# Kernel tuning notes

Hardware: AMD Instinct MI355X
Metric: run time of the kernel (lower is better)

## Reference

```python
import jax, jax.numpy as jnp
import numpy as np
from jax import lax

STRIDE = (1, 1)
PADDING = ((1, 1), (1, 1))
DILATION = (1, 1)
GROUPS = 1


def setup_inputs() -> dict:
    key = jax.random.key(0)
    k1, k2, k3, k4, k5 = jax.random.split(key, 5)
    # quantized int8-ish activations/weights stored as float (as in the torch module)
    x = jax.random.randint(k1, (32, 128, 56, 56), -128, 128).astype(jnp.float32)
    weight_int = jax.random.randint(k2, (256, 128, 3, 3), -128, 128).astype(jnp.float32)
    bias_int = jax.random.randint(k3, (256,), -1024, 1024).astype(jnp.float32)
    A = jax.random.randint(k4, (256,), 1, 32768)  # per-channel requant multiplier
    N = jax.random.randint(k5, (256,), 16, 25)    # per-channel shift
    return {
        "x": x,
        "weight_int": weight_int,
        "bias_int": bias_int,
        "A": A,
        "N": N,
        "out_min": 0,
        "out_max": 255,
    }


def reference(x, weight_int, bias_int, A, N, out_min, out_max):
    # emulate torch's x.int().float() truncation casts
    xq = jnp.trunc(x)
    wq = jnp.trunc(weight_int)
    bq = jnp.trunc(bias_int)
    out = lax.conv_general_dilated(
        xq, wq,
        window_strides=STRIDE,
        padding=PADDING,
        rhs_dilation=DILATION,
        feature_group_count=GROUPS,
        dimension_numbers=("NCHW", "OIHW", "NCHW"),
    )
    out = jnp.round(out + bq[None, :, None, None])
    # out *= A ; out >>= N  (torch float rshift == divide by 2**N)
    Af = A.astype(jnp.float32)[None, :, None, None]
    Nf = N.astype(jnp.float32)[None, :, None, None]
    out = out * Af / jnp.exp2(Nf)
    if out_min >= 0:
        out = jnp.clip(jnp.round(out), float(out_min), float(out_max))
    return out
```

## Files before the change

### kernel.cpp

```cpp
#include <hip/hip_runtime.h>
#include <stdint.h>

typedef int   v4i __attribute__((ext_vector_type(4)));
typedef float v4f __attribute__((ext_vector_type(4)));

#define XT_H_STRIDE (66*128)
#define XT_N_STRIDE (58*66*128)
#define XT_BYTES    (32*58*66*128)
#define WQ_BYTES    (256*1152)

__device__ __forceinline__ void gload16(const void* g, void* l) {
  __builtin_amdgcn_global_load_lds(
      (const __attribute__((address_space(1))) void*)g,
      (__attribute__((address_space(3))) void*)l, 16, 0, 0);
}

__global__ __launch_bounds__(256) void xform_x(const float* __restrict__ x,
                                               char* __restrict__ xt) {
  __shared__ int LB[56 * 33];
  int bid = blockIdx.x;
  int n  = bid / 58;
  int hp = bid - n * 58;
  int t  = threadIdx.x;
  int srch = hp - 1;
  bool rowok = (srch >= 0) && (srch < 56);
  char* dstrow = xt + (size_t)n * XT_N_STRIDE + (size_t)hp * XT_H_STRIDE;

  if (rowok) {
    const float* rb = x + ((size_t)(n * 128) * 56 + srch) * 56;
#pragma unroll
    for (int u0 = 0; u0 < 2; ++u0) {
      int u  = t + u0 * 256;
      int wb = u & 15;
      int cb = u >> 4;
      int w0 = wb * 4, ci0 = cb * 4;
      if (w0 < 56) {
        int dw[4] = {0, 0, 0, 0};
#pragma unroll
        for (int i = 0; i < 4; ++i) {
          v4f f = *(const v4f*)(rb + (size_t)(ci0 + i) * 3136 + w0);
#pragma unroll
          for (int j = 0; j < 4; ++j)
            dw[j] |= (((int)f[j]) & 255) << (8 * i);
        }
#pragma unroll
        for (int j = 0; j < 4; ++j)
          LB[(w0 + j) * 33 + cb] = dw[j];
      }
    }
    __syncthreads();
    for (int c = t; c < 528; c += 256) {
      int wp  = c >> 3;
      int cio = c & 7;
      int srw = wp - 1;
      v4i v = {0, 0, 0, 0};
      if (srw >= 0 && srw < 56) {
#pragma unroll
        for (int k = 0; k < 4; ++k) v[k] = LB[srw * 33 + cio * 4 + k];
      }
      *(v4i*)(dstrow + c * 16) = v;
    }
  } else {
    v4i z = {0, 0, 0, 0};
    for (int c = t; c < 528; c += 256) *(v4i*)(dstrow + c * 16) = z;
  }
}

__global__ __launch_bounds__(256) void xform_w(const float* __restrict__ wsrc,
                                               const int* __restrict__ Aq,
                                               const int* __restrict__ Nq,
                                               char* __restrict__ wq2,
                                               float* __restrict__ scale) {
  int idx = blockIdx.x * 256 + threadIdx.x;
  int co = idx / 1152;
  int k  = idx - co * 1152;
  int g  = k >> 7;
  int ci = k & 127;
  int kh = g / 3;
  int kw = g - 3 * kh;
  float f = wsrc[(size_t)(co * 128 + ci) * 9 + kh * 3 + kw];
  wq2[((k >> 6) * 256 + co) * 64 + (k & 63)] = (signed char)(int)f;
  if (idx < 256) {
    scale[idx] = (float)Aq[idx] * exp2f(-(float)Nq[idx]);
  }
}

__global__ __launch_bounds__(256, 3) void qconv_gemm(
    const char* __restrict__ xt, const char* __restrict__ wq2,
    const float* __restrict__ bias, const float* __restrict__ scale,
    const int* __restrict__ pmin, const int* __restrict__ pmax,
    float* __restrict__ out) {
  __shared__ __align__(16) char Bp[4 * 8448];

  int bid = blockIdx.x;
  int xcd = bid & 7;
  int q   = bid >> 3;
  int mt  = q & 1;
  int nt  = xcd * 112 + (q >> 1);
  int n   = nt / 28;
  int ht  = nt - n * 28;
  int h0  = ht * 2;
  int m0  = mt * 128;

  int t  = threadIdx.x;
  int wv = t >> 6;
  int ln = t & 63;
  int quad = ln >> 4;
  int l16  = ln & 15;
  int wm = wv & 1, wn = wv >> 1;

  const char* xb = xt + (size_t)n * XT_N_STRIDE + (size_t)h0 * XT_H_STRIDE;

  const char* abase = wq2 + (size_t)(m0 + wm * 64 + l16) * 64 + quad * 16;

  v4i areg[2][4];
#pragma unroll
  for (int i = 0; i < 4; ++i)
    areg[0][i] = *(const v4i*)(abase + i * 1024);

  for (int it = 0; it < 9; ++it) {
    int s = t + it * 256;
    if (s < 2112) {
      int row = s / 528;
      int rr  = s - row * 528;
      int w   = rr >> 3;
      int cq  = rr & 7;
      gload16(xb + row * XT_H_STRIDE + w * 128 + ((cq ^ (w & 7)) << 4),
              Bp + it * 4096 + wv * 1024);
    }
  }
  asm volatile("s_waitcnt vmcnt(0)" ::: "memory");
  asm volatile("s_barrier" ::: "memory");

  v4i acc[4][4];
#pragma unroll
  for (int i = 0; i < 4; ++i)
#pragma unroll
    for (int j = 0; j < 4; ++j) {
      v4i z = {0, 0, 0, 0};
      acc[i][j] = z;
    }

#pragma unroll
  for (int kt = 0; kt < 18; ++kt) {
    int cur = kt & 1;
    int p   = kt & 1;
    int g   = kt >> 1;
    int kh  = g / 3;
    int kw  = g - 3 * kh;

    if (kt < 17) {
      const char* akt = abase + ((size_t)(kt + 1) << 14);
#pragma unroll
      for (int i = 0; i < 4; ++i)
        areg[1 - cur][i] = *(const v4i*)(akt + i * 1024);
    }

    int bswz = (((p << 2) + quad) ^ ((l16 + kw) & 7)) << 4;
    const char* bbase = Bp + (wn + kh) * XT_H_STRIDE + (l16 + kw) * 128 + bswz;
    v4i b[4];
#pragma unroll
    for (int j = 0; j < 4; ++j)
      b[j] = *(const v4i*)(bbase + j * 2048);

#pragma unroll
    for (int i = 0; i < 4; ++i)
#pragma unroll
      for (int j = 0; j < 4; ++j)
        acc[i][j] = __builtin_amdgcn_mfma_i32_16x16x64_i8(areg[cur][i], b[j], acc[i][j], 0, 0, 0);
  }

  float mn = (float)pmin[0];
  float mx = (float)pmax[0];
#pragma unroll
  for (int i = 0; i < 4; ++i) {
    int co_b = m0 + wm * 64 + i * 16 + quad * 4;
#pragma unroll
    for (int r = 0; r < 4; ++r) {
      int co = co_b + r;
      float bs = bias[co];
      float sc = scale[co];
#pragma unroll
      for (int j = 0; j < 4; ++j) {
        int sl = wn * 64 + j * 16 + l16;
        int w  = sl & 63;
        int dh = sl >> 6;
        if (w < 56) {
          float f = (float)acc[i][j][r] + bs;
          f = rintf(f * sc);
          f = fminf(fmaxf(f, mn), mx);
          out[(((size_t)n * 256 + co) * 56 + (h0 + dh)) * 56 + w] = f;
        }
      }
    }
  }
}

extern "C" void kernel_launch(void* const* d_in, const int* in_sizes, int n_in,
                              void* d_out, int out_size, void* d_ws, size_t ws_size,
                              hipStream_t stream) {
  const float* x  = (const float*)d_in[0];
  const float* w  = (const float*)d_in[1];
  const float* b  = (const float*)d_in[2];
  const int*   Aq = (const int*)d_in[3];
  const int*   Nq = (const int*)d_in[4];
  const int*   mn = (const int*)d_in[5];
  const int*   mx = (const int*)d_in[6];
  float* out = (float*)d_out;

  char*  xt    = (char*)d_ws;
  char*  wq2   = xt + XT_BYTES;
  float* scale = (float*)(wq2 + WQ_BYTES);

  hipLaunchKernelGGL(xform_x, dim3(32 * 58), dim3(256), 0, stream, x, xt);
  hipLaunchKernelGGL(xform_w, dim3(1152), dim3(256), 0, stream, w, Aq, Nq, wq2, scale);
  hipLaunchKernelGGL(qconv_gemm, dim3(1792), dim3(256), 0, stream,
                     xt, wq2, b, scale, mn, mx, out);
}
```

Measured before the change: 198.2 us.

## Fuse input int8 packing into conv GEMM kernel, dropping xform_x pass

Removes the separate xform_x kernel that converted float activations into a padded, swizzled int8 NHWC workspace. Each GEMM block now zeroes its LDS tile, reads the float input rows directly, truncates and packs four channels into each 32-bit word, and writes them into the swizzled LDS layout. This saves a kernel launch and a round trip of the intermediate tensor through global memory. In exchange every block re-reads the halo rows in fp32 (4 rows per 2 output rows, across 2 M-tiles), and the async global-to-LDS loads become synchronous conversions.

```diff
diff --git a/kernel.cpp b/kernel.cpp
--- a/kernel.cpp
+++ b/kernel.cpp
@@ -4,67 +4,8 @@
 typedef int   v4i __attribute__((ext_vector_type(4)));
 typedef float v4f __attribute__((ext_vector_type(4)));
 
-#define XT_H_STRIDE (66*128)
-#define XT_N_STRIDE (58*66*128)
-#define XT_BYTES    (32*58*66*128)
-#define WQ_BYTES    (256*1152)
-
-__device__ __forceinline__ void gload16(const void* g, void* l) {
-  __builtin_amdgcn_global_load_lds(
-      (const __attribute__((address_space(1))) void*)g,
-      (__attribute__((address_space(3))) void*)l, 16, 0, 0);
-}
-
-__global__ __launch_bounds__(256) void xform_x(const float* __restrict__ x,
-                                               char* __restrict__ xt) {
-  __shared__ int LB[56 * 33];
-  int bid = blockIdx.x;
-  int n  = bid / 58;
-  int hp = bid - n * 58;
-  int t  = threadIdx.x;
-  int srch = hp - 1;
-  bool rowok = (srch >= 0) && (srch < 56);
-  char* dstrow = xt + (size_t)n * XT_N_STRIDE + (size_t)hp * XT_H_STRIDE;
-
-  if (rowok) {
-    const float* rb = x + ((size_t)(n * 128) * 56 + srch) * 56;
-#pragma unroll
-    for (int u0 = 0; u0 < 2; ++u0) {
-      int u  = t + u0 * 256;
-      int wb = u & 15;
-      int cb = u >> 4;
-      int w0 = wb * 4, ci0 = cb * 4;
-      if (w0 < 56) {
-        int dw[4] = {0, 0, 0, 0};
-#pragma unroll
-        for (int i = 0; i < 4; ++i) {
-          v4f f = *(const v4f*)(rb + (size_t)(ci0 + i) * 3136 + w0);
-#pragma unroll
-          for (int j = 0; j < 4; ++j)
-            dw[j] |= (((int)f[j]) & 255) << (8 * i);
-        }
-#pragma unroll
-        for (int j = 0; j < 4; ++j)
-          LB[(w0 + j) * 33 + cb] = dw[j];
-      }
-    }
-    __syncthreads();
-    for (int c = t; c < 528; c += 256) {
-      int wp  = c >> 3;
-      int cio = c & 7;
-      int srw = wp - 1;
-      v4i v = {0, 0, 0, 0};
-      if (srw >= 0 && srw < 56) {
-#pragma unroll
-        for (int k = 0; k < 4; ++k) v[k] = LB[srw * 33 + cio * 4 + k];
-      }
-      *(v4i*)(dstrow + c * 16) = v;
-    }
-  } else {
-    v4i z = {0, 0, 0, 0};
-    for (int c = t; c < 528; c += 256) *(v4i*)(dstrow + c * 16) = z;
-  }
-}
+#define WQ_BYTES (256*1152)
+#define BP_H     8448
 
 __global__ __launch_bounds__(256) void xform_w(const float* __restrict__ wsrc,
                                                const int* __restrict__ Aq,
@@ -86,11 +27,11 @@
 }
 
 __global__ __launch_bounds__(256, 3) void qconv_gemm(
-    const char* __restrict__ xt, const char* __restrict__ wq2,
+    const float* __restrict__ x, const char* __restrict__ wq2,
     const float* __restrict__ bias, const float* __restrict__ scale,
     const int* __restrict__ pmin, const int* __restrict__ pmax,
     float* __restrict__ out) {
-  __shared__ __align__(16) char Bp[4 * 8448];
+  __shared__ __align__(16) char Bp[4 * BP_H];
 
   int bid = blockIdx.x;
   int xcd = bid & 7;
@@ -109,7 +50,44 @@
   int l16  = ln & 15;
   int wm = wv & 1, wn = wv >> 1;
 
-  const char* xb = xt + (size_t)n * XT_N_STRIDE + (size_t)h0 * XT_H_STRIDE;
+  {
+    v4i z = {0, 0, 0, 0};
+#pragma unroll
+    for (int k = 0; k < 9; ++k) {
+      int c = t + k * 256;
+      if (c < 2112) *(v4i*)(Bp + c * 16) = z;
+    }
+  }
+  __syncthreads();
+
+  const float* xn = x + (size_t)n * 128 * 3136;
+#pragma unroll
+  for (int k = 0; k < 7; ++k) {
+    int u   = t + k * 256;
+    int r   = u / 448;
+    int rem = u - r * 448;
+    int w2  = rem >> 6;
+    int lo  = rem & 63;
+    int cd  = lo >> 1;
+    int wq  = w2 * 2 + (lo & 1);
+    int hs  = h0 - 1 + r;
+    if (hs >= 0 && hs < 56) {
+      const float* src = xn + (size_t)(cd * 4) * 3136 + hs * 56 + wq * 4;
+      int dw[4] = {0, 0, 0, 0};
+#pragma unroll
+      for (int i = 0; i < 4; ++i) {
+        v4f f = *(const v4f*)(src + (size_t)i * 3136);
+#pragma unroll
+        for (int j = 0; j < 4; ++j)
+          dw[j] |= (((int)f[j]) & 255) << (8 * i);
+      }
+#pragma unroll
+      for (int j = 0; j < 4; ++j) {
+        int wp = wq * 4 + j + 1;
+        *(int*)(Bp + r * BP_H + wp * 128 + (((cd >> 2) ^ (wp & 7)) << 4) + (cd & 3) * 4) = dw[j];
+      }
+    }
+  }
 
   const char* abase = wq2 + (size_t)(m0 + wm * 64 + l16) * 64 + quad * 16;
 
@@ -118,19 +96,7 @@
   for (int i = 0; i < 4; ++i)
     areg[0][i] = *(const v4i*)(abase + i * 1024);
 
-  for (int it = 0; it < 9; ++it) {
-    int s = t + it * 256;
-    if (s < 2112) {
-      int row = s / 528;
-      int rr  = s - row * 528;
-      int w   = rr >> 3;
-      int cq  = rr & 7;
-      gload16(xb + row * XT_H_STRIDE + w * 128 + ((cq ^ (w & 7)) << 4),
-              Bp + it * 4096 + wv * 1024);
-    }
-  }
-  asm volatile("s_waitcnt vmcnt(0)" ::: "memory");
-  asm volatile("s_barrier" ::: "memory");
+  __syncthreads();
 
   v4i acc[4][4];
 #pragma unroll
@@ -144,7 +110,6 @@
 #pragma unroll
   for (int kt = 0; kt < 18; ++kt) {
     int cur = kt & 1;
-    int p   = kt & 1;
     int g   = kt >> 1;
     int kh  = g / 3;
     int kw  = g - 3 * kh;
@@ -156,8 +121,8 @@
         areg[1 - cur][i] = *(const v4i*)(akt + i * 1024);
     }
 
-    int bswz = (((p << 2) + quad) ^ ((l16 + kw) & 7)) << 4;
-    const char* bbase = Bp + (wn + kh) * XT_H_STRIDE + (l16 + kw) * 128 + bswz;
+    int bswz = ((((kt & 1) << 2) + quad) ^ ((l16 + kw) & 7)) << 4;
+    const char* bbase = Bp + (wn + kh) * BP_H + (l16 + kw) * 128 + bswz;
     v4i b[4];
 #pragma unroll
     for (int j = 0; j < 4; ++j)
@@ -180,16 +145,16 @@
       int co = co_b + r;
       float bs = bias[co];
       float sc = scale[co];
+      float* orow = out + (((size_t)n * 256 + co) * 56 + (h0 + wn)) * 56;
 #pragma unroll
       for (int j = 0; j < 4; ++j) {
         int sl = wn * 64 + j * 16 + l16;
         int w  = sl & 63;
-        int dh = sl >> 6;
         if (w < 56) {
           float f = (float)acc[i][j][r] + bs;
           f = rintf(f * sc);
           f = fminf(fmaxf(f, mn), mx);
-          out[(((size_t)n * 256 + co) * 56 + (h0 + dh)) * 56 + w] = f;
+          orow[w] = f;
         }
       }
     }
@@ -208,12 +173,10 @@
   const int*   mx = (const int*)d_in[6];
   float* out = (float*)d_out;
 
-  char*  xt    = (char*)d_ws;
-  char*  wq2   = xt + XT_BYTES;
+  char*  wq2   = (char*)d_ws;
   float* scale = (float*)(wq2 + WQ_BYTES);
 
-  hipLaunchKernelGGL(xform_x, dim3(32 * 58), dim3(256), 0, stream, x, xt);
   hipLaunchKernelGGL(xform_w, dim3(1152), dim3(256), 0, stream, w, Aq, Nq, wq2, scale);
   hipLaunchKernelGGL(qconv_gemm, dim3(1792), dim3(256), 0, stream,
-                     xt, wq2, b, scale, mn, mx, out);
+                     x, wq2, b, scale, mn, mx, out);
 }
```

Result: slower. 208.8 us (+5.4%).
